# Kernel tuning notes

Hardware: AMD Instinct MI355X
Metric: run time of the kernel (lower is better)

The kernel has to match this reference:

```python
import jax, jax.numpy as jnp
import numpy as np

B = 8192
HID = [256, 128, 64]
OUT = 5
EPS = 1e-5

# neighbor order for branch i: all other branches in ascending index order
NEIGH = np.array([[j for j in range(8) if j != i] for i in range(8)])  # [8,7]
# adjacency gate (row,col) into A.view(-1,8,8) for branch i, neighbor slot k
# (branch 1 uses a transposed pattern for slots 3..6, exactly as in the source)
_G = [
    [(0,1),(0,2),(0,3),(4,0),(5,0),(6,0),(7,0)],
    [(0,1),(2,1),(3,1),(4,1),(5,1),(6,1),(7,1)],
    [(0,2),(1,2),(3,2),(4,2),(5,2),(6,2),(7,2)],
    [(0,3),(1,3),(2,3),(4,3),(5,3),(6,3),(7,3)],
    [(0,4),(1,4),(2,4),(3,4),(5,4),(6,4),(7,4)],
    [(0,5),(1,5),(2,5),(3,5),(4,5),(6,5),(7,5)],
    [(0,6),(1,6),(2,6),(3,6),(4,6),(5,6),(7,6)],
    [(0,7),(1,7),(2,7),(3,7),(4,7),(5,7),(6,7)],
]
GIDX = np.array([[r * 8 + c for (r, c) in row] for row in _G]).reshape(-1)  # [56]


def setup_inputs() -> dict:
    key = jax.random.key(0)
    ks = iter(jax.random.split(key, 64))
    inp = {}
    inp["state"] = jax.random.normal(next(ks), (B, 3), jnp.float32)
    for i in range(1, 9):
        inp[f"Z{i}"] = jax.random.normal(next(ks), (B, 3), jnp.float32)
    inp["A"] = jax.random.uniform(next(ks), (B, 64), jnp.float32)
    din = 3
    for l, dout in enumerate(HID):
        inp[f"W{l}"] = jax.random.normal(next(ks), (8, din, dout), jnp.float32) * 0.05
        inp[f"b{l}"] = jnp.zeros((8, dout), jnp.float32)
        inp[f"g{l}"] = jnp.ones((8, dout), jnp.float32)
        inp[f"be{l}"] = jnp.zeros((8, dout), jnp.float32)
        inp[f"Wg{l}"] = jax.random.normal(next(ks), (8, 7 * din, 7), jnp.float32) * 0.05
        inp[f"bg{l}"] = jnp.zeros((8, 7), jnp.float32)
        din = dout
    inp["Wout"] = jax.random.normal(next(ks), (8, din, OUT), jnp.float32) * 0.05
    inp["bout"] = jnp.zeros((8, OUT), jnp.float32)
    return inp


def _forward(Z, A, layers, Wout, bout):
    # Z: [B,8,D0], A: [B,64]
    b = Z.shape[0]
    gates = A[:, jnp.asarray(GIDX)].reshape(b, 8, 7)  # [B,8,7]
    neigh = jnp.asarray(NEIGH)
    for (W, bias, g, be, Wg, bg) in layers:
        Zn = Z[:, neigh, :]                                   # [B,8,7,D]
        Zall = Zn.reshape(b, 8, -1)                           # [B,8,7D]
        a = jax.nn.softmax(jnp.einsum('bif,ifo->bio', Zall, Wg) + bg, axis=-1)
        NZ = jnp.einsum('bik,bikd->bid', a * gates, Zn)       # attention-weighted neighbor sum
        h = jnp.einsum('bid,ido->bio', Z + NZ, W) + bias
        mu = h.mean(-1, keepdims=True)
        var = ((h - mu) ** 2).mean(-1, keepdims=True)
        h = (h - mu) / jnp.sqrt(var + EPS) * g + be           # per-branch LayerNorm
        Z = jax.nn.relu(h)
    return jnp.tanh(jnp.einsum('bid,ido->bio', Z, Wout) + bout)  # [B,8,5]


def reference(state, Z1, Z2, Z3, Z4, Z5, Z6, Z7, Z8, A,
              W0, b0, g0, be0, Wg0, bg0,
              W1, b1, g1, be1, Wg1, bg1,
              W2, b2, g2, be2, Wg2, bg2,
              Wout, bout):
    Z = jnp.stack([Z1, Z2, Z3, Z4, Z5, Z6, Z7, Z8], axis=1)  # [B,8,3]
    layers = [(W0, b0, g0, be0, Wg0, bg0),
              (W1, b1, g1, be1, Wg1, bg1),
              (W2, b2, g2, be2, Wg2, bg2)]
    return _forward(Z, A, layers, Wout, bout)
```

## Files before the change

kernel.cpp:

```cpp
#include <hip/hip_runtime.h>
#include <math.h>

typedef _Float16 v8h __attribute__((ext_vector_type(8)));
typedef float    v4f __attribute__((ext_vector_type(4)));

#define NB    32
#define DSTR  264
#define WSTR  68
#define EPSLN 1e-5f

struct KP {
  const float* Z[8];
  const float* A;
  const float *W0, *b0, *g0, *be0, *Wg0, *bg0;
  const float *b1, *g1, *be1, *bg1;
  const float *b2, *g2, *be2, *bg2;
  const float *bout;
  const _Float16 *WgT1, *WgT2, *WT1, *WT2, *WoT;
  float* out;
};

__device__ __forceinline__ void cvt_one(const float* __restrict__ src, _Float16* __restrict__ dst,
                                        int F, int Osrc, int Opad, int t) {
  const int f  = t % F;
  const int io = t / F;
  const int o  = io % Opad;
  const int i  = io / Opad;
  dst[t] = (o < Osrc) ? (_Float16)src[(i * F + f) * Osrc + o] : (_Float16)0.f;
}

#define E1 114688
#define E2 57344
#define E3 4096
#define E4 262144
#define E5 65536

__global__ void cvt_all(const float* __restrict__ Wg1, const float* __restrict__ Wg2,
                        const float* __restrict__ Wout, const float* __restrict__ W1,
                        const float* __restrict__ W2, _Float16* __restrict__ ws) {
  int t = blockIdx.x * 256 + threadIdx.x;
  if (t < E1) { cvt_one(Wg1, ws, 1792, 7, 8, t); return; }
  t -= E1;
  if (t < E2) { cvt_one(Wg2, ws + E1, 896, 7, 8, t); return; }
  t -= E2;
  if (t < E3) { cvt_one(Wout, ws + E1 + E2, 64, 5, 8, t); return; }
  t -= E3;
  if (t < E4) { cvt_one(W1, ws + E1 + E2 + E3, 256, 128, 128, t); return; }
  t -= E4;
  if (t < E5) { cvt_one(W2, ws + E1 + E2 + E3 + E4, 128, 64, 64, t); return; }
}

template<int D, int O, int NPRE>
__device__ __forceinline__ void mfma_layer(
    _Float16* __restrict__ zh, float* __restrict__ wbuf, const float* __restrict__ gbuf,
    const v8h* gpre,
    const _Float16* __restrict__ WgT, const float* __restrict__ bg,
    const _Float16* __restrict__ WT, const float* __restrict__ bias,
    const float* __restrict__ g, const float* __restrict__ be,
    const _Float16* __restrict__ preBase, int preStride, v8h* pre,
    int i, int q, int r)
{
  constexpr int KS = D / 32;
  constexpr int NT = O / 16;

  const _Float16* WgB = WgT + (size_t)(i * 8 + r) * (7 * D) + q * 8;
  const _Float16* WB  = WT  + (size_t)(i * O + r) * D + q * 8;

  v8h dbf[NT];
  #pragma unroll
  for (int n = 0; n < NT; ++n) dbf[n] = *(const v8h*)(WB + (size_t)n * 16 * D);

  v8h gbf[7];
  #pragma unroll
  for (int nb = 0; nb < 7; ++nb) gbf[nb] = gpre[nb];

  v4f ca[2][2];
  #pragma unroll
  for (int mt = 0; mt < 2; ++mt)
    #pragma unroll
    for (int c = 0; c < 2; ++c) ca[mt][c] = (v4f){0.f,0.f,0.f,0.f};

  #pragma unroll
  for (int ks = 0; ks < KS; ++ks) {
    const int d0 = ks * 32 + q * 8;
    v8h gbn[7];
    if (ks + 1 < KS) {
      #pragma unroll
      for (int nb = 0; nb < 7; ++nb)
        gbn[nb] = *(const v8h*)(WgB + nb * D + (ks + 1) * 32);
    }
    #pragma unroll
    for (int nb = 0; nb < 7; ++nb) {
      const int nk = nb + (nb >= i);
      const v8h af0 = *(const v8h*)(zh + (nk * NB + r) * DSTR + d0);
      const v8h af1 = *(const v8h*)(zh + (nk * NB + 16 + r) * DSTR + d0);
      ca[0][nb & 1] = __builtin_amdgcn_mfma_f32_16x16x32_f16(af0, gbf[nb], ca[0][nb & 1], 0, 0, 0);
      ca[1][nb & 1] = __builtin_amdgcn_mfma_f32_16x16x32_f16(af1, gbf[nb], ca[1][nb & 1], 0, 0, 0);
    }
    if (ks + 1 < KS) {
      #pragma unroll
      for (int nb = 0; nb < 7; ++nb) gbf[nb] = gbn[nb];
    }
  }
  const v4f gacc[2] = { ca[0][0] + ca[0][1], ca[1][0] + ca[1][1] };

  const float bgv = (r < 7) ? bg[i * 7 + r] : 0.f;
  #pragma unroll
  for (int mt = 0; mt < 2; ++mt) {
    #pragma unroll
    for (int reg = 0; reg < 4; ++reg) {
      const float v = gacc[mt][reg] + bgv;
      float m = (r < 7) ? v : -3.0e38f;
      #pragma unroll
      for (int mk = 1; mk < 16; mk <<= 1) m = fmaxf(m, __shfl_xor(m, mk, 16));
      const float e = (r < 7) ? __expf(v - m) : 0.f;
      float s = e;
      #pragma unroll
      for (int mk = 1; mk < 16; mk <<= 1) s += __shfl_xor(s, mk, 16);
      const int b = mt * 16 + q * 4 + reg;
      if (r < 7) wbuf[b * WSTR + i * 8 + r] = (e / s) * gbuf[b * WSTR + i * 8 + r];
    }
  }

  v4f acc[2][NT];
  #pragma unroll
  for (int mt = 0; mt < 2; ++mt)
    #pragma unroll
    for (int n = 0; n < NT; ++n) acc[mt][n] = (v4f){0.f,0.f,0.f,0.f};

  _Float16 wh[2][7];
  #pragma unroll
  for (int mt = 0; mt < 2; ++mt)
    #pragma unroll
    for (int nb = 0; nb < 7; ++nb)
      wh[mt][nb] = (_Float16)wbuf[(mt * 16 + r) * WSTR + i * 8 + nb];

  #pragma unroll
  for (int ks = 0; ks < KS; ++ks) {
    const int d0 = ks * 32 + q * 8;
    v8h dbn[NT];
    if (ks + 1 < KS) {
      #pragma unroll
      for (int n = 0; n < NT; ++n)
        dbn[n] = *(const v8h*)(WB + (size_t)n * 16 * D + (ks + 1) * 32);
    }
    v8h x01[2];
    #pragma unroll
    for (int mt = 0; mt < 2; ++mt) {
      v8h zn[7];
      #pragma unroll
      for (int nb = 0; nb < 7; ++nb) {
        const int nk = nb + (nb >= i);
        zn[nb] = *(const v8h*)(zh + ((nk * NB + mt * 16 + r) * DSTR + d0));
      }
      v8h x = *(const v8h*)(zh + ((i * NB + mt * 16 + r) * DSTR + d0));
      x = (x + (zn[0] * wh[mt][0] + zn[1] * wh[mt][1]))
        + ((zn[2] * wh[mt][2] + zn[3] * wh[mt][3])
        + ((zn[4] * wh[mt][4] + zn[5] * wh[mt][5]) + zn[6] * wh[mt][6]));
      x01[mt] = x;
    }
    #pragma unroll
    for (int n = 0; n < NT; ++n) {
      acc[0][n] = __builtin_amdgcn_mfma_f32_16x16x32_f16(x01[0], dbf[n], acc[0][n], 0, 0, 0);
      acc[1][n] = __builtin_amdgcn_mfma_f32_16x16x32_f16(x01[1], dbf[n], acc[1][n], 0, 0, 0);
    }
    if (ks + 1 < KS) {
      #pragma unroll
      for (int n = 0; n < NT; ++n) dbf[n] = dbn[n];
    }
  }

  #pragma unroll
  for (int t = 0; t < NPRE; ++t)
    pre[t] = *(const v8h*)(preBase + (size_t)t * preStride);

  float bv[NT], gv[NT], bev[NT];
  #pragma unroll
  for (int n = 0; n < NT; ++n) {
    const int o = n * 16 + r;
    bv[n] = bias[i * O + o]; gv[n] = g[i * O + o]; bev[n] = be[i * O + o];
  }
  #pragma unroll
  for (int mt = 0; mt < 2; ++mt) {
    #pragma unroll
    for (int reg = 0; reg < 4; ++reg) {
      float s1 = 0.f, s2 = 0.f;
      #pragma unroll
      for (int n = 0; n < NT; ++n) {
        const float h = acc[mt][n][reg] + bv[n];
        acc[mt][n][reg] = h;
        s1 += h; s2 += h * h;
      }
      #pragma unroll
      for (int mk = 1; mk < 16; mk <<= 1) { s1 += __shfl_xor(s1, mk, 16); s2 += __shfl_xor(s2, mk, 16); }
      const float mean = s1 * (1.f / O);
      const float var  = s2 * (1.f / O) - mean * mean;
      const float rs   = rsqrtf(var + EPSLN);
      #pragma unroll
      for (int n = 0; n < NT; ++n) {
        const float h = (acc[mt][n][reg] - mean) * rs * gv[n] + bev[n];
        acc[mt][n][reg] = fmaxf(h, 0.f);
      }
    }
  }
  __syncthreads();
  #pragma unroll
  for (int mt = 0; mt < 2; ++mt)
    #pragma unroll
    for (int n = 0; n < NT; ++n)
      #pragma unroll
      for (int reg = 0; reg < 4; ++reg) {
        const int b = mt * 16 + q * 4 + reg;
        zh[(i * NB + b) * DSTR + n * 16 + r] = (_Float16)acc[mt][n][reg];
      }
  __syncthreads();
}

__launch_bounds__(512, 2)
__global__ void actor_mfma(KP p)
{
  __shared__ __align__(16) _Float16 zh[8 * NB * DSTR];
  __shared__ float wbuf[NB * WSTR];
  __shared__ float gbuf[NB * WSTR];
  __shared__ float xbuf[8 * NB * 4];

  const int i = threadIdx.x >> 6;
  const int u = threadIdx.x & 63;
  const int q = u >> 4, r = u & 15;
  const int bbase = blockIdx.x * NB;

  {
    #pragma unroll
    for (int c = 0; c < 2; ++c) {
      const int idx = c * 64 + u;
      if (idx < NB * 3) {
        const int b = idx / 3, d = idx - 3 * (idx / 3);
        zh[(i * NB + b) * DSTR + d] = (_Float16)p.Z[i][(size_t)(bbase + b) * 3 + d];
      }
    }
    for (int t = threadIdx.x; t < NB * 64; t += 512) {
      const int b = t >> 6, ik = t & 63;
      const int ii = ik >> 3, k = ik & 7;
      if (k < 7) {
        const int j = k + (k >= ii);
        const int gidx = (ii == 0 && j <= 3) ? j : 8 * j + ii;
        gbuf[b * WSTR + ik] = p.A[(size_t)(bbase + b) * 64 + gidx];
      }
    }
  }
  __syncthreads();

  for (int c = 0; c < NB / 8; ++c) {
    const int b = c * 8 + (u >> 3), o8 = u & 7;
    float v = -3.0e38f;
    if (o8 < 7) {
      v = p.bg0[i * 7 + o8];
      #pragma unroll
      for (int k = 0; k < 7; ++k) {
        const int nk = k + (k >= i);
        const _Float16* zp = zh + (nk * NB + b) * DSTR;
        const float* wp = p.Wg0 + (i * 21 + k * 3) * 7 + o8;
        v += (float)zp[0] * wp[0] + (float)zp[1] * wp[7] + (float)zp[2] * wp[14];
      }
    }
    float m = v;
    #pragma unroll
    for (int mk = 1; mk < 8; mk <<= 1) m = fmaxf(m, __shfl_xor(m, mk, 8));
    const float e = (o8 < 7) ? __expf(v - m) : 0.f;
    float s = e;
    #pragma unroll
    for (int mk = 1; mk < 8; mk <<= 1) s += __shfl_xor(s, mk, 8);
    if (o8 < 7) wbuf[b * WSTR + i * 8 + o8] = (e / s) * gbuf[b * WSTR + i * 8 + o8];
  }
  #pragma unroll
  for (int c = 0; c < 2; ++c) {
    const int idx = c * 64 + u;
    if (idx < NB * 3) {
      const int b = idx / 3, d = idx - 3 * (idx / 3);
      float x = (float)zh[(i * NB + b) * DSTR + d];
      #pragma unroll
      for (int k = 0; k < 7; ++k) {
        const int nk = k + (k >= i);
        x += wbuf[b * WSTR + i * 8 + k] * (float)zh[(nk * NB + b) * DSTR + d];
      }
      xbuf[(i * NB + b) * 4 + d] = x;
    }
  }
  v8h gpre1[7];
  {
    const _Float16* gb = p.WgT1 + (size_t)(i * 8 + r) * (7 * 256) + q * 8;
    #pragma unroll
    for (int nb = 0; nb < 7; ++nb) gpre1[nb] = *(const v8h*)(gb + nb * 256);
  }
  __syncthreads();
  {
    const int bh = u >> 5, lo = u & 31, o = lo * 8;
    float w0r[3][8], b0r[8], g0r[8], be0r[8];
    #pragma unroll
    for (int d = 0; d < 3; ++d)
      #pragma unroll
      for (int j = 0; j < 8; ++j) w0r[d][j] = p.W0[(i * 3 + d) * 256 + o + j];
    #pragma unroll
    for (int j = 0; j < 8; ++j) {
      b0r[j] = p.b0[i * 256 + o + j];
      g0r[j] = p.g0[i * 256 + o + j];
      be0r[j] = p.be0[i * 256 + o + j];
    }
    for (int it = 0; it < NB / 2; ++it) {
      const int b = it * 2 + bh;
      const float x0 = xbuf[(i * NB + b) * 4 + 0];
      const float x1 = xbuf[(i * NB + b) * 4 + 1];
      const float x2 = xbuf[(i * NB + b) * 4 + 2];
      float h[8], s1 = 0.f, s2 = 0.f;
      #pragma unroll
      for (int j = 0; j < 8; ++j) {
        const float v = b0r[j] + x0 * w0r[0][j] + x1 * w0r[1][j] + x2 * w0r[2][j];
        h[j] = v; s1 += v; s2 += v * v;
      }
      #pragma unroll
      for (int mk = 1; mk < 32; mk <<= 1) { s1 += __shfl_xor(s1, mk, 32); s2 += __shfl_xor(s2, mk, 32); }
      const float mean = s1 * (1.f / 256.f);
      const float var  = s2 * (1.f / 256.f) - mean * mean;
      const float rs   = rsqrtf(var + EPSLN);
      v8h hv;
      #pragma unroll
      for (int j = 0; j < 8; ++j)
        hv[j] = (_Float16)fmaxf((h[j] - mean) * rs * g0r[j] + be0r[j], 0.f);
      *(v8h*)(zh + (i * NB + b) * DSTR + o) = hv;
    }
  }
  __syncthreads();

  v8h gpre2[7], wpre[8];
  mfma_layer<256, 128, 7>(zh, wbuf, gbuf, gpre1, p.WgT1, p.bg1, p.WT1, p.b1, p.g1, p.be1,
                          p.WgT2 + (size_t)(i * 8 + r) * (7 * 128) + q * 8, 128, gpre2, i, q, r);
  mfma_layer<128, 64, 8>(zh, wbuf, gbuf, gpre2, p.WgT2, p.bg2, p.WT2, p.b2, p.g2, p.be2,
                         p.WoT + (size_t)(i * 8 + (u & 7)) * 64, 8, wpre, i, q, r);

  {
    const int b8 = u >> 3, o8 = u & 7;
    const float bo = (o8 < 5) ? p.bout[i * 5 + o8] : 0.f;
    for (int c = 0; c < NB / 8; ++c) {
      const int b = c * 8 + b8;
      const _Float16* zp = zh + (i * NB + b) * DSTR;
      float acc = bo;
      #pragma unroll
      for (int t8 = 0; t8 < 8; ++t8) {
        const v8h z8 = *(const v8h*)(zp + t8 * 8);
        #pragma unroll
        for (int j = 0; j < 8; ++j) acc += (float)z8[j] * (float)wpre[t8][j];
      }
      if (o8 < 5)
        p.out[((size_t)(bbase + b) * 8 + i) * 5 + o8] = tanhf(acc);
    }
  }
}

extern "C" void kernel_launch(void* const* d_in, const int* in_sizes, int n_in,
                              void* d_out, int out_size, void* d_ws, size_t ws_size,
                              hipStream_t stream) {
  KP p;
  for (int i = 0; i < 8; ++i) p.Z[i] = (const float*)d_in[1 + i];
  p.A   = (const float*)d_in[9];
  p.W0  = (const float*)d_in[10]; p.b0 = (const float*)d_in[11];
  p.g0  = (const float*)d_in[12]; p.be0 = (const float*)d_in[13];
  p.Wg0 = (const float*)d_in[14]; p.bg0 = (const float*)d_in[15];
  const float* W1  = (const float*)d_in[16]; p.b1 = (const float*)d_in[17];
  p.g1  = (const float*)d_in[18]; p.be1 = (const float*)d_in[19];
  const float* Wg1 = (const float*)d_in[20]; p.bg1 = (const float*)d_in[21];
  const float* W2  = (const float*)d_in[22]; p.b2 = (const float*)d_in[23];
  p.g2  = (const float*)d_in[24]; p.be2 = (const float*)d_in[25];
  const float* Wg2 = (const float*)d_in[26]; p.bg2 = (const float*)d_in[27];
  const float* Wout = (const float*)d_in[28]; p.bout = (const float*)d_in[29];
  p.out = (float*)d_out;

  _Float16* wsH = (_Float16*)d_ws;
  p.WgT1 = wsH;
  p.WgT2 = wsH + E1;
  p.WoT  = wsH + E1 + E2;
  p.WT1  = wsH + E1 + E2 + E3;
  p.WT2  = wsH + E1 + E2 + E3 + E4;

  const int total = E1 + E2 + E3 + E4 + E5;
  hipLaunchKernelGGL(cvt_all, dim3((total + 255) / 256), dim3(256), 0, stream,
                     Wg1, Wg2, Wout, W1, W2, wsH);

  hipLaunchKernelGGL(actor_mfma, dim3(8192 / NB), dim3(512), 0, stream, p);
}
```

Measured before the change: 75.70 us.

## Compute layer-0 LayerNorm stats analytically and move layer-0 and output GEMMs to MFMA

```diff
diff --git a/kernel.cpp b/kernel.cpp
--- a/kernel.cpp
+++ b/kernel.cpp
@@ -16,7 +16,8 @@
   const float *b1, *g1, *be1, *bg1;
   const float *b2, *g2, *be2, *bg2;
   const float *bout;
-  const _Float16 *WgT1, *WgT2, *WT1, *WT2, *WoT;
+  const _Float16 *WgT1, *WgT2, *WT1, *WT2, *WoT, *W0T;
+  const float *stats;
   float* out;
 };
 
@@ -34,10 +35,13 @@
 #define E3 4096
 #define E4 262144
 #define E5 65536
+#define E6 65536
+#define NSTAT 136
 
 __global__ void cvt_all(const float* __restrict__ Wg1, const float* __restrict__ Wg2,
                         const float* __restrict__ Wout, const float* __restrict__ W1,
-                        const float* __restrict__ W2, _Float16* __restrict__ ws) {
+                        const float* __restrict__ W2, const float* __restrict__ W0,
+                        const float* __restrict__ b0, _Float16* __restrict__ ws) {
   int t = blockIdx.x * 256 + threadIdx.x;
   if (t < E1) { cvt_one(Wg1, ws, 1792, 7, 8, t); return; }
   t -= E1;
@@ -48,6 +52,36 @@
   if (t < E4) { cvt_one(W1, ws + E1 + E2 + E3, 256, 128, 128, t); return; }
   t -= E4;
   if (t < E5) { cvt_one(W2, ws + E1 + E2 + E3 + E4, 128, 64, 64, t); return; }
+  t -= E5;
+  if (t < E6) {
+    const int k = t & 31;
+    const int o = (t >> 5) & 255;
+    const int i = t >> 13;
+    ws[E1 + E2 + E3 + E4 + E5 + t] = (k < 3) ? (_Float16)W0[(i * 3 + k) * 256 + o] : (_Float16)0.f;
+    return;
+  }
+  t -= E6;
+  if (t < NSTAT) {
+    float* sf = (float*)(ws + E1 + E2 + E3 + E4 + E5 + E6);
+    const int i = t / 17, j = t % 17;
+    float v = 0.f;
+    if (j < 3) {
+      for (int o = 0; o < 256; ++o) v += W0[(i * 3 + j) * 256 + o];
+    } else if (j == 3) {
+      for (int o = 0; o < 256; ++o) v += b0[i * 256 + o];
+    } else if (j < 13) {
+      const int a = (j - 4) / 3, bb = (j - 4) % 3;
+      for (int o = 0; o < 256; ++o)
+        v += W0[(i * 3 + a) * 256 + o] * W0[(i * 3 + bb) * 256 + o];
+    } else if (j < 16) {
+      const int d = j - 13;
+      for (int o = 0; o < 256; ++o)
+        v += W0[(i * 3 + d) * 256 + o] * b0[i * 256 + o];
+    } else {
+      for (int o = 0; o < 256; ++o) { const float x = b0[i * 256 + o]; v += x * x; }
+    }
+    sf[t] = v * (1.f / 256.f);
+  }
 }
 
 template<int D, int O, int NPRE>
@@ -229,7 +263,12 @@
   const int q = u >> 4, r = u & 15;
   const int bbase = blockIdx.x * NB;
 
+  float w0g[21];
   {
+    const int o8c = (u & 7) < 7 ? (u & 7) : 6;
+    #pragma unroll
+    for (int kd = 0; kd < 21; ++kd) w0g[kd] = p.Wg0[(i * 21 + kd) * 7 + o8c];
+
     #pragma unroll
     for (int c = 0; c < 2; ++c) {
       const int idx = c * 64 + u;
@@ -250,27 +289,30 @@
   }
   __syncthreads();
 
-  for (int c = 0; c < NB / 8; ++c) {
-    const int b = c * 8 + (u >> 3), o8 = u & 7;
-    float v = -3.0e38f;
-    if (o8 < 7) {
-      v = p.bg0[i * 7 + o8];
-      #pragma unroll
-      for (int k = 0; k < 7; ++k) {
-        const int nk = k + (k >= i);
-        const _Float16* zp = zh + (nk * NB + b) * DSTR;
-        const float* wp = p.Wg0 + (i * 21 + k * 3) * 7 + o8;
-        v += (float)zp[0] * wp[0] + (float)zp[1] * wp[7] + (float)zp[2] * wp[14];
-      }
-    }
-    float m = v;
-    #pragma unroll
-    for (int mk = 1; mk < 8; mk <<= 1) m = fmaxf(m, __shfl_xor(m, mk, 8));
-    const float e = (o8 < 7) ? __expf(v - m) : 0.f;
-    float s = e;
-    #pragma unroll
-    for (int mk = 1; mk < 8; mk <<= 1) s += __shfl_xor(s, mk, 8);
-    if (o8 < 7) wbuf[b * WSTR + i * 8 + o8] = (e / s) * gbuf[b * WSTR + i * 8 + o8];
+  {
+    const float bgv0 = ((u & 7) < 7) ? p.bg0[i * 7 + (u & 7)] : 0.f;
+    for (int c = 0; c < NB / 8; ++c) {
+      const int b = c * 8 + (u >> 3), o8 = u & 7;
+      float v = -3.0e38f;
+      if (o8 < 7) {
+        v = bgv0;
+        #pragma unroll
+        for (int k = 0; k < 7; ++k) {
+          const int nk = k + (k >= i);
+          const _Float16* zp = zh + (nk * NB + b) * DSTR;
+          v += (float)zp[0] * w0g[k * 3 + 0] + (float)zp[1] * w0g[k * 3 + 1]
+             + (float)zp[2] * w0g[k * 3 + 2];
+        }
+      }
+      float m = v;
+      #pragma unroll
+      for (int mk = 1; mk < 8; mk <<= 1) m = fmaxf(m, __shfl_xor(m, mk, 8));
+      const float e = (o8 < 7) ? __expf(v - m) : 0.f;
+      float s = e;
+      #pragma unroll
+      for (int mk = 1; mk < 8; mk <<= 1) s += __shfl_xor(s, mk, 8);
+      if (o8 < 7) wbuf[b * WSTR + i * 8 + o8] = (e / s) * gbuf[b * WSTR + i * 8 + o8];
+    }
   }
   #pragma unroll
   for (int c = 0; c < 2; ++c) {
@@ -292,66 +334,92 @@
     #pragma unroll
     for (int nb = 0; nb < 7; ++nb) gpre1[nb] = *(const v8h*)(gb + nb * 256);
   }
+  float st[17];
+  #pragma unroll
+  for (int s = 0; s < 17; ++s) st[s] = p.stats[i * 17 + s];
+  float b0v[16], g0v[16], be0v[16];
+  #pragma unroll
+  for (int n = 0; n < 16; ++n) {
+    const int o = n * 16 + r;
+    b0v[n] = p.b0[i * 256 + o]; g0v[n] = p.g0[i * 256 + o]; be0v[n] = p.be0[i * 256 + o];
+  }
   __syncthreads();
   {
-    const int bh = u >> 5, lo = u & 31, o = lo * 8;
-    float w0r[3][8], b0r[8], g0r[8], be0r[8];
-    #pragma unroll
-    for (int d = 0; d < 3; ++d)
-      #pragma unroll
-      for (int j = 0; j < 8; ++j) w0r[d][j] = p.W0[(i * 3 + d) * 256 + o + j];
-    #pragma unroll
-    for (int j = 0; j < 8; ++j) {
-      b0r[j] = p.b0[i * 256 + o + j];
-      g0r[j] = p.g0[i * 256 + o + j];
-      be0r[j] = p.be0[i * 256 + o + j];
-    }
-    for (int it = 0; it < NB / 2; ++it) {
-      const int b = it * 2 + bh;
-      const float x0 = xbuf[(i * NB + b) * 4 + 0];
-      const float x1 = xbuf[(i * NB + b) * 4 + 1];
-      const float x2 = xbuf[(i * NB + b) * 4 + 2];
-      float h[8], s1 = 0.f, s2 = 0.f;
-      #pragma unroll
-      for (int j = 0; j < 8; ++j) {
-        const float v = b0r[j] + x0 * w0r[0][j] + x1 * w0r[1][j] + x2 * w0r[2][j];
-        h[j] = v; s1 += v; s2 += v * v;
-      }
-      #pragma unroll
-      for (int mk = 1; mk < 32; mk <<= 1) { s1 += __shfl_xor(s1, mk, 32); s2 += __shfl_xor(s2, mk, 32); }
-      const float mean = s1 * (1.f / 256.f);
-      const float var  = s2 * (1.f / 256.f) - mean * mean;
-      const float rs   = rsqrtf(var + EPSLN);
-      v8h hv;
-      #pragma unroll
-      for (int j = 0; j < 8; ++j)
-        hv[j] = (_Float16)fmaxf((h[j] - mean) * rs * g0r[j] + be0r[j], 0.f);
-      *(v8h*)(zh + (i * NB + b) * DSTR + o) = hv;
+    float mu8[8], rs8[8];
+    #pragma unroll
+    for (int mt = 0; mt < 2; ++mt)
+      #pragma unroll
+      for (int reg = 0; reg < 4; ++reg) {
+        const int row = mt * 16 + q * 4 + reg;
+        const float x0 = xbuf[(i * NB + row) * 4 + 0];
+        const float x1 = xbuf[(i * NB + row) * 4 + 1];
+        const float x2 = xbuf[(i * NB + row) * 4 + 2];
+        const float mu = st[3] + x0 * st[0] + x1 * st[1] + x2 * st[2];
+        const float ex2 = st[16] + 2.f * (x0 * st[13] + x1 * st[14] + x2 * st[15])
+                        + x0 * (x0 * st[4] + 2.f * (x1 * st[5] + x2 * st[6]))
+                        + x1 * (x1 * st[8] + 2.f * (x2 * st[9]))
+                        + x2 * x2 * st[12];
+        mu8[mt * 4 + reg] = mu;
+        rs8[mt * 4 + reg] = rsqrtf(fmaxf(ex2 - mu * mu, 0.f) + EPSLN);
+      }
+    v8h af[2];
+    #pragma unroll
+    for (int j = 0; j < 8; ++j) { af[0][j] = (_Float16)0.f; af[1][j] = (_Float16)0.f; }
+    if (q == 0) {
+      #pragma unroll
+      for (int mt = 0; mt < 2; ++mt)
+        #pragma unroll
+        for (int j = 0; j < 3; ++j)
+          af[mt][j] = (_Float16)xbuf[(i * NB + mt * 16 + r) * 4 + j];
+    }
+    const _Float16* WB0 = p.W0T + (size_t)(i * 256 + r) * 32 + q * 8;
+    #pragma unroll
+    for (int nt = 0; nt < 16; ++nt) {
+      const v8h bf = *(const v8h*)(WB0 + (size_t)nt * 16 * 32);
+      const float bo = b0v[nt];
+      v4f a0 = (v4f){bo, bo, bo, bo}, a1 = a0;
+      a0 = __builtin_amdgcn_mfma_f32_16x16x32_f16(af[0], bf, a0, 0, 0, 0);
+      a1 = __builtin_amdgcn_mfma_f32_16x16x32_f16(af[1], bf, a1, 0, 0, 0);
+      const int o = nt * 16 + r;
+      #pragma unroll
+      for (int reg = 0; reg < 4; ++reg) {
+        const float h0 = (a0[reg] - mu8[reg])     * rs8[reg]     * g0v[nt] + be0v[nt];
+        const float h1 = (a1[reg] - mu8[4 + reg]) * rs8[4 + reg] * g0v[nt] + be0v[nt];
+        zh[(i * NB + q * 4 + reg) * DSTR + o]      = (_Float16)fmaxf(h0, 0.f);
+        zh[(i * NB + 16 + q * 4 + reg) * DSTR + o] = (_Float16)fmaxf(h1, 0.f);
+      }
     }
   }
   __syncthreads();
 
-  v8h gpre2[7], wpre[8];
+  v8h gpre2[7], wpre[2];
   mfma_layer<256, 128, 7>(zh, wbuf, gbuf, gpre1, p.WgT1, p.bg1, p.WT1, p.b1, p.g1, p.be1,
                           p.WgT2 + (size_t)(i * 8 + r) * (7 * 128) + q * 8, 128, gpre2, i, q, r);
-  mfma_layer<128, 64, 8>(zh, wbuf, gbuf, gpre2, p.WgT2, p.bg2, p.WT2, p.b2, p.g2, p.be2,
-                         p.WoT + (size_t)(i * 8 + (u & 7)) * 64, 8, wpre, i, q, r);
+  mfma_layer<128, 64, 2>(zh, wbuf, gbuf, gpre2, p.WgT2, p.bg2, p.WT2, p.b2, p.g2, p.be2,
+                         p.WoT + (size_t)(i * 8 + r) * 64 + q * 8, 32, wpre, i, q, r);
 
   {
-    const int b8 = u >> 3, o8 = u & 7;
-    const float bo = (o8 < 5) ? p.bout[i * 5 + o8] : 0.f;
-    for (int c = 0; c < NB / 8; ++c) {
-      const int b = c * 8 + b8;
-      const _Float16* zp = zh + (i * NB + b) * DSTR;
-      float acc = bo;
-      #pragma unroll
-      for (int t8 = 0; t8 < 8; ++t8) {
-        const v8h z8 = *(const v8h*)(zp + t8 * 8);
+    const float bo = (r < 5) ? p.bout[i * 5 + r] : 0.f;
+    v4f oacc[2];
+    oacc[0] = (v4f){bo, bo, bo, bo}; oacc[1] = oacc[0];
+    #pragma unroll
+    for (int ks = 0; ks < 2; ++ks) {
+      const int d0 = ks * 32 + q * 8;
+      const v8h a0 = *(const v8h*)(zh + (i * NB + r) * DSTR + d0);
+      const v8h a1 = *(const v8h*)(zh + (i * NB + 16 + r) * DSTR + d0);
+      oacc[0] = __builtin_amdgcn_mfma_f32_16x16x32_f16(a0, wpre[ks], oacc[0], 0, 0, 0);
+      oacc[1] = __builtin_amdgcn_mfma_f32_16x16x32_f16(a1, wpre[ks], oacc[1], 0, 0, 0);
+    }
+    if (r < 5) {
+      #pragma unroll
+      for (int mt = 0; mt < 2; ++mt)
         #pragma unroll
-        for (int j = 0; j < 8; ++j) acc += (float)z8[j] * (float)wpre[t8][j];
-      }
-      if (o8 < 5)
-        p.out[((size_t)(bbase + b) * 8 + i) * 5 + o8] = tanhf(acc);
+        for (int reg = 0; reg < 4; ++reg) {
+          const int b = mt * 16 + q * 4 + reg;
+          const float x = oacc[mt][reg];
+          const float ex = __expf(2.f * x);
+          p.out[((size_t)(bbase + b) * 8 + i) * 5 + r] = 1.f - 2.f / (ex + 1.f);
+        }
     }
   }
 }
@@ -380,10 +448,12 @@
   p.WoT  = wsH + E1 + E2;
   p.WT1  = wsH + E1 + E2 + E3;
   p.WT2  = wsH + E1 + E2 + E3 + E4;
-
-  const int total = E1 + E2 + E3 + E4 + E5;
+  p.W0T  = wsH + E1 + E2 + E3 + E4 + E5;
+  p.stats = (const float*)(wsH + E1 + E2 + E3 + E4 + E5 + E6);
+
+  const int total = E1 + E2 + E3 + E4 + E5 + E6 + NSTAT;
   hipLaunchKernelGGL(cvt_all, dim3((total + 255) / 256), dim3(256), 0, stream,
-                     Wg1, Wg2, Wout, W1, W2, wsH);
+                     Wg1, Wg2, Wout, W1, W2, p.W0, p.b0, wsH);
 
   hipLaunchKernelGGL(actor_mfma, dim3(8192 / NB), dim3(512), 0, stream, p);
 }
```

Result: slower. 81.36 us (+7.5%).
